# Optimization experiments

Measured on AMD Instinct MI355X. Metric: run time of the kernel, lower is better.

## Reference

```python
import jax, jax.numpy as jnp
from jax import lax
import numpy as np

B, T, K = 256, 1024, 64


def setup_inputs() -> dict:
    key = jax.random.key(0)
    k1, k2, k3 = jax.random.split(key, 3)
    emissions = jax.random.normal(k1, (B, T, K), dtype=jnp.float32)
    tag_ids = jax.random.randint(k2, (B, T), 0, K, dtype=jnp.int32)
    mask = jnp.ones((B, T), dtype=bool)
    transition_weight = jax.random.normal(k3, (K, K), dtype=jnp.float32)
    return {"emissions": emissions, "tag_ids": tag_ids, "mask": mask,
            "transition_weight": transition_weight}


def _crf_log_likelihood(emissions, tags, mask, trans):
    # emissions: [B,T,K], tags/mask: [B,T], trans: [K,K]
    maskf = mask.astype(emissions.dtype)
    # sequence score: unary emissions at gold tags + pairwise transitions
    unary = jnp.take_along_axis(emissions, tags[..., None], axis=2)[..., 0]  # [B,T]
    unary_score = jnp.sum(unary * maskf, axis=1)
    trans_score = jnp.sum(trans[tags[:, :-1], tags[:, 1:]] * maskf[:, 1:], axis=1)
    seq_score = unary_score + trans_score  # [B]
    # log partition via forward (alpha) recursion over time
    def step(alpha, xs):
        e_t, m_t = xs  # [B,K], [B]
        new = jax.nn.logsumexp(alpha[:, :, None] + trans[None], axis=1) + e_t
        alpha = jnp.where(m_t[:, None], new, alpha)  # carry through padding
        return alpha, None
    alpha0 = emissions[:, 0]
    em_t = jnp.swapaxes(emissions, 0, 1)[1:]  # [T-1,B,K]
    m_t = jnp.swapaxes(mask, 0, 1)[1:]        # [T-1,B]
    alpha, _ = lax.scan(step, alpha0, (em_t, m_t))
    log_z = jax.nn.logsumexp(alpha, axis=1)  # [B]
    return seq_score - log_z


def _crf_decode(emissions, mask, trans):
    # Viterbi: forward max recursion with backpointers, then backtrack.
    num_tags = emissions.shape[-1]
    ident = jnp.arange(num_tags, dtype=jnp.int32)[None, :]  # identity bp for padding

    def fstep(delta, xs):
        e_t, m_t = xs  # [B,K], [B]
        scores = delta[:, :, None] + trans[None]  # [B,K_prev,K_cur]
        bp = jnp.argmax(scores, axis=1).astype(jnp.int32)  # [B,K]
        new = jnp.max(scores, axis=1) + e_t
        delta = jnp.where(m_t[:, None], new, delta)
        bp = jnp.where(m_t[:, None], bp, ident)
        return delta, bp

    delta0 = emissions[:, 0]
    em_t = jnp.swapaxes(emissions, 0, 1)[1:]
    m_t = jnp.swapaxes(mask, 0, 1)[1:]
    delta, bps = lax.scan(fstep, delta0, (em_t, m_t))  # bps: [T-1,B,K]
    last_tag = jnp.argmax(delta, axis=1).astype(jnp.int32)  # [B]

    def bstep(tag, bp_t):
        prev = jnp.take_along_axis(bp_t, tag[:, None], axis=1)[:, 0]
        return prev, tag

    first_tag, tags_rest = lax.scan(bstep, last_tag, bps, reverse=True)
    decoded = jnp.concatenate([first_tag[:, None], jnp.swapaxes(tags_rest, 0, 1)], axis=1)
    return decoded  # [B,T]


def reference(emissions, tag_ids, mask, transition_weight):
    ll = _crf_log_likelihood(emissions, tag_ids, mask, transition_weight)
    loss = -jnp.mean(ll)
    decoded = _crf_decode(emissions, mask, transition_weight)
    mask_i = mask.astype(jnp.int32)
    tag_accuracy = (jnp.sum((decoded == tag_ids).astype(jnp.int32) * mask_i)
                    / jnp.sum(mask_i))
    decoded_masked = decoded * mask_i  # padded positions zeroed (ragged stand-in)
    return loss, decoded_masked, tag_accuracy
```

## Files before the change

### kernel.cpp

```cpp
#include <hip/hip_runtime.h>

#define BB 256
#define TT 1024
#define KK 64
#define CS 65


__device__ __forceinline__ float rlane(float x, int i) {
  return __int_as_float(__builtin_amdgcn_readlane(__float_as_int(x), i));
}
#define RL(S, i) rlane(S, i)

__device__ __forceinline__ float wavemax(float v) {
#pragma unroll
  for (int off = 1; off <= 32; off <<= 1) v = fmaxf(v, __shfl_xor(v, off));
  return v;
}

#define CFQ4(S, a, b, c, d) \
  q0 = __builtin_fmaf(RL(S, a), Ecol[eb + (a)], q0); \
  q1 = __builtin_fmaf(RL(S, b), Ecol[eb + (b)], q1); \
  q2 = __builtin_fmaf(RL(S, c), Ecol[eb + (c)], q2); \
  q3 = __builtin_fmaf(RL(S, d), Ecol[eb + (d)], q3);
#define CFQALL(S) \
  CFQ4(S, 0, 1, 2, 3)     CFQ4(S, 4, 5, 6, 7)     CFQ4(S, 8, 9, 10, 11) \
  CFQ4(S, 12, 13, 14, 15) CFQ4(S, 16, 17, 18, 19) CFQ4(S, 20, 21, 22, 23) \
  CFQ4(S, 24, 25, 26, 27) CFQ4(S, 28, 29, 30, 31) CFQ4(S, 32, 33, 34, 35) \
  CFQ4(S, 36, 37, 38, 39) CFQ4(S, 40, 41, 42, 43) CFQ4(S, 44, 45, 46, 47) \
  CFQ4(S, 48, 49, 50, 51) CFQ4(S, 52, 53, 54, 55) CFQ4(S, 56, 57, 58, 59) \
  CFQ4(S, 60, 61, 62, 63)

#define CFWD_STEP(T_, E_, M_) { \
  int eb = jb65; asm volatile("" : "+v"(eb)); \
  float q0 = 0.f, q1 = 0.f, q2 = 0.f, q3 = 0.f; \
  CFQALL(x) \
  float q = (q0 + q1) + (q2 + q3); \
  q *= (E_); \
  q = (M_) ? q : x; \
  if (((T_) & 7) == 0) { \
    float gm = wavemax(x); \
    q *= __builtin_amdgcn_rcpf(gm); \
    offset += __logf(gm); \
  } \
  x = q; }

#define CVQ(g, a, b, c, d) float vm##g; { \
  float v0 = RL(x, a) + Ccol[cb + (a)]; \
  float v1 = RL(x, b) + Ccol[cb + (b)]; \
  float v2 = RL(x, c) + Ccol[cb + (c)]; \
  float v3 = RL(x, d) + Ccol[cb + (d)]; \
  vm##g = fmaxf(fmaxf(v0, v1), fmaxf(v2, v3)); }

#define CVIT_STEP(T_, E_, M_) { \
  int cb = jb65; asm volatile("" : "+v"(cb)); \
  CVQ(0, 0, 1, 2, 3)      CVQ(1, 4, 5, 6, 7)      CVQ(2, 8, 9, 10, 11) \
  CVQ(3, 12, 13, 14, 15)  CVQ(4, 16, 17, 18, 19)  CVQ(5, 20, 21, 22, 23) \
  CVQ(6, 24, 25, 26, 27)  CVQ(7, 28, 29, 30, 31)  CVQ(8, 32, 33, 34, 35) \
  CVQ(9, 36, 37, 38, 39)  CVQ(10, 40, 41, 42, 43) CVQ(11, 44, 45, 46, 47) \
  CVQ(12, 48, 49, 50, 51) CVQ(13, 52, 53, 54, 55) CVQ(14, 56, 57, 58, 59) \
  CVQ(15, 60, 61, 62, 63) \
  float b0 = fmaxf(vm0, vm1),   b1 = fmaxf(vm2, vm3); \
  float b2 = fmaxf(vm4, vm5),   b3 = fmaxf(vm6, vm7); \
  float b4 = fmaxf(vm8, vm9),   b5 = fmaxf(vm10, vm11); \
  float b6 = fmaxf(vm12, vm13), b7 = fmaxf(vm14, vm15); \
  float best = fmaxf(fmaxf(fmaxf(b0, b1), fmaxf(b2, b3)), \
                     fmaxf(fmaxf(b4, b5), fmaxf(b6, b7))); \
  float nd = (M_) ? (best + (E_)) : x; \
  x = nd; }

#define AG(i0, i1, i2, i3, i4, i5, i6, i7) { \
  float v0 = RL(x2, i0) + Ccol[db + (i0)]; \
  float v1 = RL(x2, i1) + Ccol[db + (i1)]; \
  float v2 = RL(x2, i2) + Ccol[db + (i2)]; \
  float v3 = RL(x2, i3) + Ccol[db + (i3)]; \
  float v4 = RL(x2, i4) + Ccol[db + (i4)]; \
  float v5 = RL(x2, i5) + Ccol[db + (i5)]; \
  float v6 = RL(x2, i6) + Ccol[db + (i6)]; \
  float v7 = RL(x2, i7) + Ccol[db + (i7)]; \
  bool p0 = v1 > v0; float a0 = p0 ? v1 : v0; int n0 = p0 ? (i1) : (i0); \
  bool p1 = v3 > v2; float a1 = p1 ? v3 : v2; int n1 = p1 ? (i3) : (i2); \
  bool p2 = v5 > v4; float a2 = p2 ? v5 : v4; int n2 = p2 ? (i5) : (i4); \
  bool p3 = v7 > v6; float a3 = p3 ? v7 : v6; int n3 = p3 ? (i7) : (i6); \
  bool r0 = a1 > a0; float bb0 = r0 ? a1 : a0; int m0 = r0 ? n1 : n0; \
  bool r1 = a3 > a2; float bb1 = r1 ? a3 : a2; int m1 = r1 ? n3 : n2; \
  bool s0 = bb1 > bb0; float gg = s0 ? bb1 : bb0; int w0 = s0 ? m1 : m0; \
  bool u0 = gg > bv; bv = u0 ? gg : bv; bi = u0 ? w0 : bi; }

#define FG(A,B,C,D,E0,E1,E2,E3,OP) \
  "v_readlane_b32 s56, %[x], " #A "\n\t" \
  "v_readlane_b32 s57, %[x], " #B "\n\t" \
  "v_readlane_b32 s58, %[x], " #C "\n\t" \
  "v_readlane_b32 s59, %[x], " #D "\n\t" \
  #OP " v20, s56, v" #E0 "\n\t" \
  #OP " v21, s57, v" #E1 "\n\t" \
  #OP " v22, s58, v" #E2 "\n\t" \
  #OP " v23, s59, v" #E3 "\n\t"

#define FWD_DOT \
  FG(0,1,2,3,64,65,66,67,v_mul_f32)      FG(4,5,6,7,68,69,70,71,v_fmac_f32) \
  FG(8,9,10,11,72,73,74,75,v_fmac_f32)   FG(12,13,14,15,76,77,78,79,v_fmac_f32) \
  FG(16,17,18,19,80,81,82,83,v_fmac_f32) FG(20,21,22,23,84,85,86,87,v_fmac_f32) \
  FG(24,25,26,27,88,89,90,91,v_fmac_f32) FG(28,29,30,31,92,93,94,95,v_fmac_f32) \
  FG(32,33,34,35,96,97,98,99,v_fmac_f32) FG(36,37,38,39,100,101,102,103,v_fmac_f32) \
  FG(40,41,42,43,104,105,106,107,v_fmac_f32) FG(44,45,46,47,108,109,110,111,v_fmac_f32) \
  FG(48,49,50,51,112,113,114,115,v_fmac_f32) FG(52,53,54,55,116,117,118,119,v_fmac_f32) \
  FG(56,57,58,59,120,121,122,123,v_fmac_f32) FG(60,61,62,63,124,125,126,127,v_fmac_f32)

#define VG(A,B,C,D,E0,E1,E2,E3,RED) \
  "v_readlane_b32 s56, %[x], " #A "\n\t" \
  "v_readlane_b32 s57, %[x], " #B "\n\t" \
  "v_readlane_b32 s58, %[x], " #C "\n\t" \
  "v_readlane_b32 s59, %[x], " #D "\n\t" \
  "v_add_f32 v16, s56, v" #E0 "\n\t" \
  "v_add_f32 v17, s57, v" #E1 "\n\t" \
  "v_add_f32 v18, s58, v" #E2 "\n\t" \
  "v_add_f32 v19, s59, v" #E3 "\n\t" \
  "v_max3_f32 v16, v16, v17, v18\n\t" \
  RED "\n\t"

#define VIT_DOT \
  VG(0,1,2,3,64,65,66,67,"v_max_f32 v20, v16, v19") \
  VG(4,5,6,7,68,69,70,71,"v_max3_f32 v20, v20, v16, v19") \
  VG(8,9,10,11,72,73,74,75,"v_max3_f32 v20, v20, v16, v19") \
  VG(12,13,14,15,76,77,78,79,"v_max3_f32 v20, v20, v16, v19") \
  VG(16,17,18,19,80,81,82,83,"v_max3_f32 v20, v20, v16, v19") \
  VG(20,21,22,23,84,85,86,87,"v_max3_f32 v20, v20, v16, v19") \
  VG(24,25,26,27,88,89,90,91,"v_max3_f32 v20, v20, v16, v19") \
  VG(28,29,30,31,92,93,94,95,"v_max3_f32 v20, v20, v16, v19") \
  VG(32,33,34,35,96,97,98,99,"v_max3_f32 v20, v20, v16, v19") \
  VG(36,37,38,39,100,101,102,103,"v_max3_f32 v20, v20, v16, v19") \
  VG(40,41,42,43,104,105,106,107,"v_max3_f32 v20, v20, v16, v19") \
  VG(44,45,46,47,108,109,110,111,"v_max3_f32 v20, v20, v16, v19") \
  VG(48,49,50,51,112,113,114,115,"v_max3_f32 v20, v20, v16, v19") \
  VG(52,53,54,55,116,117,118,119,"v_max3_f32 v20, v20, v16, v19") \
  VG(56,57,58,59,120,121,122,123,"v_max3_f32 v20, v20, v16, v19") \
  VG(60,61,62,63,124,125,126,127,"v_max3_f32 v20, v20, v16, v19")

#define AGLD(N,OFF) "global_load_dword v" #N ", v13, %[tp] offset:" #OFF "\n\t"
#define AGLE(N,OFF) "global_load_dword v" #N ", v12, %[ep] offset:" #OFF "\n\t"
#define AGLM(N,OFF) "global_load_dword v" #N ", v14, %[mp] offset:" #OFF "\n\t"

#define ELOADS \
  AGLD(64,0) AGLD(65,256) AGLD(66,512) AGLD(67,768) AGLD(68,1024) AGLD(69,1280) \
  AGLD(70,1536) AGLD(71,1792) AGLD(72,2048) AGLD(73,2304) AGLD(74,2560) AGLD(75,2816) \
  AGLD(76,3072) AGLD(77,3328) AGLD(78,3584) AGLD(79,3840) \
  "v_add_u32 v13, 0x1000, v13\n\t" \
  AGLD(80,0) AGLD(81,256) AGLD(82,512) AGLD(83,768) AGLD(84,1024) AGLD(85,1280) \
  AGLD(86,1536) AGLD(87,1792) AGLD(88,2048) AGLD(89,2304) AGLD(90,2560) AGLD(91,2816) \
  AGLD(92,3072) AGLD(93,3328) AGLD(94,3584) AGLD(95,3840) \
  "v_add_u32 v13, 0x1000, v13\n\t" \
  AGLD(96,0) AGLD(97,256) AGLD(98,512) AGLD(99,768) AGLD(100,1024) AGLD(101,1280) \
  AGLD(102,1536) AGLD(103,1792) AGLD(104,2048) AGLD(105,2304) AGLD(106,2560) AGLD(107,2816) \
  AGLD(108,3072) AGLD(109,3328) AGLD(110,3584) AGLD(111,3840) \
  "v_add_u32 v13, 0x1000, v13\n\t" \
  AGLD(112,0) AGLD(113,256) AGLD(114,512) AGLD(115,768) AGLD(116,1024) AGLD(117,1280) \
  AGLD(118,1536) AGLD(119,1792) AGLD(120,2048) AGLD(121,2304) AGLD(122,2560) AGLD(123,2816) \
  AGLD(124,3072) AGLD(125,3328) AGLD(126,3584) AGLD(127,3840)

#define AMUL(N) "v_mul_f32 v" #N ", 0x3fb8aa3b, v" #N "\n\t"
#define AEXI(N) "v_exp_f32 v" #N ", v" #N "\n\t"
#define EEXPALL \
  AMUL(64) AMUL(65) AMUL(66) AMUL(67) AMUL(68) AMUL(69) AMUL(70) AMUL(71) \
  AMUL(72) AMUL(73) AMUL(74) AMUL(75) AMUL(76) AMUL(77) AMUL(78) AMUL(79) \
  AMUL(80) AMUL(81) AMUL(82) AMUL(83) AMUL(84) AMUL(85) AMUL(86) AMUL(87) \
  AMUL(88) AMUL(89) AMUL(90) AMUL(91) AMUL(92) AMUL(93) AMUL(94) AMUL(95) \
  AMUL(96) AMUL(97) AMUL(98) AMUL(99) AMUL(100) AMUL(101) AMUL(102) AMUL(103) \
  AMUL(104) AMUL(105) AMUL(106) AMUL(107) AMUL(108) AMUL(109) AMUL(110) AMUL(111) \
  AMUL(112) AMUL(113) AMUL(114) AMUL(115) AMUL(116) AMUL(117) AMUL(118) AMUL(119) \
  AMUL(120) AMUL(121) AMUL(122) AMUL(123) AMUL(124) AMUL(125) AMUL(126) AMUL(127) \
  AEXI(64) AEXI(65) AEXI(66) AEXI(67) AEXI(68) AEXI(69) AEXI(70) AEXI(71) \
  AEXI(72) AEXI(73) AEXI(74) AEXI(75) AEXI(76) AEXI(77) AEXI(78) AEXI(79) \
  AEXI(80) AEXI(81) AEXI(82) AEXI(83) AEXI(84) AEXI(85) AEXI(86) AEXI(87) \
  AEXI(88) AEXI(89) AEXI(90) AEXI(91) AEXI(92) AEXI(93) AEXI(94) AEXI(95) \
  AEXI(96) AEXI(97) AEXI(98) AEXI(99) AEXI(100) AEXI(101) AEXI(102) AEXI(103) \
  AEXI(104) AEXI(105) AEXI(106) AEXI(107) AEXI(108) AEXI(109) AEXI(110) AEXI(111) \
  AEXI(112) AEXI(113) AEXI(114) AEXI(115) AEXI(116) AEXI(117) AEXI(118) AEXI(119) \
  AEXI(120) AEXI(121) AEXI(122) AEXI(123) AEXI(124) AEXI(125) AEXI(126) AEXI(127)

#define EMIS16 \
  AGLE(40,0) AGLE(41,256) AGLE(42,512) AGLE(43,768) AGLE(44,1024) AGLE(45,1280) \
  AGLE(46,1536) AGLE(47,1792) AGLE(48,2048) AGLE(49,2304) AGLE(50,2560) AGLE(51,2816) \
  AGLE(52,3072) AGLE(53,3328) AGLE(54,3584) AGLE(55,3840)
#define EMIS8 \
  AGLE(40,0) AGLE(41,256) AGLE(42,512) AGLE(43,768) AGLE(44,1024) AGLE(45,1280) \
  AGLE(46,1536) AGLE(47,1792)
#define MASK16 \
  AGLM(128,0) AGLM(129,4) AGLM(130,8) AGLM(131,12) AGLM(132,16) AGLM(133,20) \
  AGLM(134,24) AGLM(135,28) AGLM(136,32) AGLM(137,36) AGLM(138,40) AGLM(139,44) \
  AGLM(140,48) AGLM(141,52) AGLM(142,56) AGLM(143,60)
#define MASK8 \
  AGLM(128,0) AGLM(129,4) AGLM(130,8) AGLM(131,12) AGLM(132,16) AGLM(133,20) \
  AGLM(134,24) AGLM(135,28)

#define AEM(D,R) "v_mul_f32 v" #D ", 0x3fb8aa3b, v" #R "\n\t"
#define EMEXP16 \
  AEM(24,40) AEM(25,41) AEM(26,42) AEM(27,43) AEM(28,44) AEM(29,45) AEM(30,46) AEM(31,47) \
  AEM(32,48) AEM(33,49) AEM(34,50) AEM(35,51) AEM(36,52) AEM(37,53) AEM(38,54) AEM(39,55) \
  AEXI(24) AEXI(25) AEXI(26) AEXI(27) AEXI(28) AEXI(29) AEXI(30) AEXI(31) \
  AEXI(32) AEXI(33) AEXI(34) AEXI(35) AEXI(36) AEXI(37) AEXI(38) AEXI(39)
#define EMEXP8 \
  AEM(24,40) AEM(25,41) AEM(26,42) AEM(27,43) AEM(28,44) AEM(29,45) AEM(30,46) AEM(31,47) \
  AEXI(24) AEXI(25) AEXI(26) AEXI(27) AEXI(28) AEXI(29) AEXI(30) AEXI(31)

#define AFSTEP(MR,EV) \
  "v_cmp_ne_u32 vcc, 0, v" #MR "\n\t" \
  FWD_DOT \
  "v_add_f32 v16, v20, v21\n\t" \
  "v_add_f32 v17, v22, v23\n\t" \
  "v_add_f32 v16, v16, v17\n\t" \
  "v_mul_f32 v16, v16, v" #EV "\n\t" \
  "v_cndmask_b32 %[x], %[x], v16, vcc\n\t"

#define RNRM \
  "v_mov_b32 v17, %[x]\n\t" \
  "ds_swizzle_b32 v18, v17 offset:0x041F\n\t" \
  "s_waitcnt lgkmcnt(0)\n\t" \
  "v_max_f32 v17, v17, v18\n\t" \
  "ds_swizzle_b32 v18, v17 offset:0x081F\n\t" \
  "s_waitcnt lgkmcnt(0)\n\t" \
  "v_max_f32 v17, v17, v18\n\t" \
  "ds_swizzle_b32 v18, v17 offset:0x101F\n\t" \
  "s_waitcnt lgkmcnt(0)\n\t" \
  "v_max_f32 v17, v17, v18\n\t" \
  "ds_swizzle_b32 v18, v17 offset:0x201F\n\t" \
  "s_waitcnt lgkmcnt(0)\n\t" \
  "v_max_f32 v17, v17, v18\n\t" \
  "ds_swizzle_b32 v18, v17 offset:0x401F\n\t" \
  "s_waitcnt lgkmcnt(0)\n\t" \
  "v_max_f32 v17, v17, v18\n\t" \
  "v_readlane_b32 s56, v17, 0\n\t" \
  "v_readlane_b32 s57, v17, 32\n\t" \
  "v_mov_b32 v18, s57\n\t" \
  "v_max_f32 v18, s56, v18\n\t" \
  "v_readlane_b32 s56, v18, 0\n\t"

#define AFSTEPR(MR,EV) \
  "v_cmp_ne_u32 vcc, 0, v" #MR "\n\t" \
  FWD_DOT \
  "v_add_f32 v16, v20, v21\n\t" \
  "v_add_f32 v17, v22, v23\n\t" \
  "v_add_f32 v16, v16, v17\n\t" \
  "v_mul_f32 v16, v16, v" #EV "\n\t" \
  RNRM \
  "v_cndmask_b32 %[x], %[x], v16, vcc\n\t" \
  "v_rcp_f32 v18, s56\n\t" \
  "v_log_f32 v19, s56\n\t" \
  "v_mul_f32 %[x], %[x], v18\n\t" \
  "v_fmac_f32 %[off], 0x3f317218, v19\n\t"

#define AVSTEP(MR,EV) \
  "v_cmp_ne_u32 vcc, 0, v" #MR "\n\t" \
  VIT_DOT \
  "v_add_f32 v16, v20, v" #EV "\n\t" \
  "v_cndmask_b32 %[x], %[x], v16, vcc\n\t"

#define CLOBS \
  "v11","v12","v13","v14","v16","v17","v18","v19","v20","v21","v22","v23", \
  "v24","v25","v26","v27","v28","v29","v30","v31","v32","v33","v34","v35", \
  "v36","v37","v38","v39","v40","v41","v42","v43","v44","v45","v46","v47", \
  "v48","v49","v50","v51","v52","v53","v54","v55", \
  "v64","v65","v66","v67","v68","v69","v70","v71","v72","v73","v74","v75", \
  "v76","v77","v78","v79","v80","v81","v82","v83","v84","v85","v86","v87", \
  "v88","v89","v90","v91","v92","v93","v94","v95","v96","v97","v98","v99", \
  "v100","v101","v102","v103","v104","v105","v106","v107","v108","v109", \
  "v110","v111","v112","v113","v114","v115","v116","v117","v118","v119", \
  "v120","v121","v122","v123","v124","v125","v126","v127","v128","v129", \
  "v130","v131","v132","v133","v134","v135","v136","v137","v138","v139", \
  "v140","v141","v142","v143", \
  "s55","s56","s57","s58","s59","vcc","scc","memory"

__global__ __launch_bounds__(512)
__attribute__((amdgpu_waves_per_eu(1, 2)))
void crf_mega_kernel(
    const float* __restrict__ em, const int* __restrict__ mask,
    const float* __restrict__ trans, const int* __restrict__ tags,
    float* __restrict__ out_dec, float* ll_sum, int* match, int* maskSum) {

  __shared__ float Ecol[KK * CS];
  __shared__ float Ccol[KK * CS];
  __shared__ __align__(16) float ckw[64][KK];
  __shared__ float fin[KK];
  __shared__ unsigned char mrow[TT];
  __shared__ unsigned char bpl[TT][KK];
  __shared__ unsigned char segm[32][KK];
  __shared__ unsigned char bs[40];
  __shared__ int redm[32];

  const int b = blockIdx.x;
  const int tid = threadIdx.x;
  const int wv = tid >> 6;
  const int j = tid & 63;
  const int jb65 = j * CS;

  const float* emb = em + (size_t)b * TT * KK;
  const int* mb = mask + (size_t)b * TT;
  const int* tgb = tags + (size_t)b * TT;

  for (int t = tid; t < TT; t += 512) mrow[t] = (unsigned char)(mb[t] ? 1 : 0);
  if (wv == 0) {
#pragma unroll 4
    for (int i = 0; i < KK; ++i) Ecol[jb65 + i] = __expf(trans[i * KK + j]);
  } else if (wv == 1) {
#pragma unroll 4
    for (int i = 0; i < KK; ++i) Ccol[jb65 + i] = trans[i * KK + j];
  }
  __syncthreads();

  if (wv == 0) {
    float raw = emb[j];
    float x, offset;
    {
      float m0 = wavemax(raw);
      offset = m0;
      float s = __expf(raw - m0);
      int eb = jb65; asm volatile("" : "+v"(eb));
      float q0 = 0.f, q1 = 0.f, q2 = 0.f, q3 = 0.f;
      CFQALL(s)
      float q = (q0 + q1) + (q2 + q3);
      q *= __expf(emb[KK + j]);
      x = mrow[1] ? q : s;
    }
    for (int t = 2; t <= 7; ++t) {
      float e = __expf(emb[(size_t)t * KK + j]);
      int m = mrow[t];
      CFWD_STEP(t, e, m)
    }
    asm volatile(
      "s_mov_b32 s55, 0\n\t"
      "v_mov_b32 v12, %[vo]\n\t"
      "v_mov_b32 v13, %[jo]\n\t"
      "v_mov_b32 v14, 32\n\t"
      ELOADS
      "s_waitcnt vmcnt(0)\n\t"
      EEXPALL
      "9:\n\t"
      MASK16
      EMIS16
      "v_add_u32 v12, 0x1000, v12\n\t"
      "v_add_u32 v14, 64, v14\n\t"
      "s_waitcnt vmcnt(0)\n\t"
      EMEXP16
      AFSTEPR(128,24) AFSTEP(129,25) AFSTEP(130,26) AFSTEP(131,27)
      AFSTEP(132,28)  AFSTEP(133,29) AFSTEP(134,30) AFSTEP(135,31)
      AFSTEPR(136,32) AFSTEP(137,33) AFSTEP(138,34) AFSTEP(139,35)
      AFSTEP(140,36)  AFSTEP(141,37) AFSTEP(142,38) AFSTEP(143,39)
      "s_add_u32 s55, s55, 1\n\t"
      "s_cmp_lt_u32 s55, 63\n\t"
      "s_cbranch_scc1 9b\n\t"
      MASK8
      EMIS8
      "s_waitcnt vmcnt(0)\n\t"
      EMEXP8
      AFSTEPR(128,24) AFSTEP(129,25) AFSTEP(130,26) AFSTEP(131,27)
      AFSTEP(132,28)  AFSTEP(133,29) AFSTEP(134,30) AFSTEP(135,31)
      "s_waitcnt vmcnt(0) lgkmcnt(0)\n\t"
      : [x]"+v"(x), [off]"+v"(offset)
      : [ep]"s"(emb), [mp]"s"(mb), [tp]"s"(trans),
        [vo]"v"(2048 + 4 * j), [jo]"v"(4 * j)
      : CLOBS);

    float ssum = x;
#pragma unroll
    for (int off = 1; off <= 32; off <<= 1) ssum += __shfl_xor(ssum, off);
    if (tid == 0) atomicAdd(ll_sum, -(offset + __logf(ssum)));

  } else if (wv == 1) {
    float x = emb[j];
    unsigned ckoff = (unsigned)(unsigned long long)(&ckw[1][j]);
    asm volatile(
      "s_mov_b32 s55, 0\n\t"
      "v_mov_b32 v11, %[ck]\n\t"
      "v_mov_b32 v12, %[vo]\n\t"
      "v_mov_b32 v13, %[jo]\n\t"
      "v_mov_b32 v14, 4\n\t"
      ELOADS
      "s_waitcnt vmcnt(0)\n\t"
      "8:\n\t"
      MASK16
      EMIS16
      "v_add_u32 v12, 0x1000, v12\n\t"
      "v_add_u32 v14, 64, v14\n\t"
      "s_waitcnt vmcnt(0)\n\t"
      AVSTEP(128,40) AVSTEP(129,41) AVSTEP(130,42) AVSTEP(131,43)
      AVSTEP(132,44) AVSTEP(133,45) AVSTEP(134,46) AVSTEP(135,47)
      AVSTEP(136,48) AVSTEP(137,49) AVSTEP(138,50) AVSTEP(139,51)
      AVSTEP(140,52) AVSTEP(141,53) AVSTEP(142,54) AVSTEP(143,55)
      "ds_write_b32 v11, %[x]\n\t"
      "v_add_u32 v11, 0x100, v11\n\t"
      "s_add_u32 s55, s55, 1\n\t"
      "s_cmp_lt_u32 s55, 63\n\t"
      "s_cbranch_scc1 8b\n\t"
      MASK8
      EMIS8
      "s_waitcnt vmcnt(0)\n\t"
      AVSTEP(128,40) AVSTEP(129,41) AVSTEP(130,42) AVSTEP(131,43)
      AVSTEP(132,44) AVSTEP(133,45) AVSTEP(134,46) AVSTEP(135,47)
      "s_waitcnt vmcnt(0) lgkmcnt(0)\n\t"
      : [x]"+v"(x)
      : [ep]"s"(emb), [mp]"s"(mb), [tp]"s"(trans),
        [vo]"v"(256 + 4 * j), [jo]"v"(4 * j), [ck]"v"(ckoff)
      : CLOBS);
    for (int t = TT - 7; t <= TT - 1; ++t) {
      float e = emb[(size_t)t * KK + j];
      int m = mrow[t];
      CVIT_STEP(t, e, m)
    }
    fin[j] = x;

  } else if (wv == 2) {
    float acc = 0.f;
    int cnt = 0;
    for (int t = j; t < TT; t += 64) {
      if (mb[t]) {
        int tg = tgb[t];
        acc += emb[(size_t)t * KK + tg];
        cnt += 1;
        if (t >= 1) acc += trans[tgb[t - 1] * KK + tg];
      }
    }
#pragma unroll
    for (int off = 1; off <= 32; off <<= 1) {
      acc += __shfl_xor(acc, off);
      cnt += __shfl_xor(cnt, off);
    }
    if (j == 0) { atomicAdd(ll_sum, acc); atomicAdd(maskSum, cnt); }
  }

  __syncthreads();

#pragma unroll 1
  for (int kk = 0; kk < 4; ++kk) {
    int s = wv + 8 * kk;
    int tS = 32 * s + 1;
    int tE = (s == 31) ? (TT - 1) : (32 * s + 32);
    float x2 = (s == 0) ? emb[j] : ckw[2 * s][j];
    float e_nx = emb[(size_t)tS * KK + j];
#pragma unroll 1
    for (int t = tS; t <= tE; ++t) {
      float e = e_nx;
      if (t < tE) e_nx = emb[(size_t)(t + 1) * KK + j];
      int db = jb65; asm volatile("" : "+v"(db));
      float bv = -__builtin_inff(); int bi = 0;
      AG(0, 1, 2, 3, 4, 5, 6, 7)        AG(8, 9, 10, 11, 12, 13, 14, 15)
      AG(16, 17, 18, 19, 20, 21, 22, 23) AG(24, 25, 26, 27, 28, 29, 30, 31)
      AG(32, 33, 34, 35, 36, 37, 38, 39) AG(40, 41, 42, 43, 44, 45, 46, 47)
      AG(48, 49, 50, 51, 52, 53, 54, 55) AG(56, 57, 58, 59, 60, 61, 62, 63)
      int m = mrow[t];
      float nd = m ? (bv + e) : x2;
      int bp = m ? bi : j;
      bpl[t][j] = (unsigned char)bp;
      x2 = nd;
    }
  }
  __syncthreads();

  {
    int j0 = tid & 63;
    int sg = tid >> 6;
    int xs[4]; int tS[4], tE[4];
#pragma unroll
    for (int kk = 0; kk < 4; ++kk) {
      int s = sg + 8 * kk;
      xs[kk] = j0;
      tS[kk] = 32 * s + 1;
      tE[kk] = (s == 31) ? (TT - 1) : (32 * s + 32);
    }
    for (int q = 0; q < 32; ++q) {
#pragma unroll
      for (int kk = 0; kk < 4; ++kk) {
        int t = tE[kk] - q;
        if (t >= tS[kk]) xs[kk] = bpl[t][xs[kk]];
      }
    }
#pragma unroll
    for (int kk = 0; kk < 4; ++kk) segm[sg + 8 * kk][j0] = (unsigned char)xs[kk];
  }
  __syncthreads();

  if (tid == 0) {
    float bd = fin[0];
    int lt = 0;
    for (int i = 1; i < KK; ++i) {
      float v2 = fin[i];
      if (v2 > bd) { bd = v2; lt = i; }
    }
    bs[32] = (unsigned char)lt;
    for (int s = 31; s >= 0; --s) bs[s] = segm[s][bs[s + 1]];
  }
  __syncthreads();

  if (tid < 32) {
    int s = tid;
    int x = bs[s + 1];
    int cnt = 0;
    int tEnd = (s == 31) ? (TT - 1) : (32 * s + 32);
    if (s == 31) {
      int m = mrow[TT - 1];
      out_dec[(size_t)b * TT + TT - 1] = (float)(m ? x : 0);
      cnt += (m && x == tgb[TT - 1]);
    }
    for (int t = tEnd; t >= 32 * s + 1; --t) {
      x = bpl[t][x];
      int m2 = mrow[t - 1];
      out_dec[(size_t)b * TT + t - 1] = (float)(m2 ? x : 0);
      cnt += (m2 && x == tgb[t - 1]);
    }
    redm[s] = cnt;
  }
  __syncthreads();
  if (tid == 0) {
    int c = 0;
    for (int s = 0; s < 32; ++s) c += redm[s];
    atomicAdd(match, c);
  }
}

__global__ void finalize_kernel(const float* ll_sum, const int* match,
                                const int* maskSum, float* d_out) {
  d_out[0] = -(*ll_sum) / (float)BB;
  d_out[1 + BB * TT] = (float)(*match) / (float)(*maskSum);
}

extern "C" void kernel_launch(void* const* d_in, const int* in_sizes, int n_in,
                              void* d_out, int out_size, void* d_ws, size_t ws_size,
                              hipStream_t stream) {
  const float* em = (const float*)d_in[0];
  const int* tags = (const int*)d_in[1];
  const int* mask = (const int*)d_in[2];
  const float* trans = (const float*)d_in[3];
  float* out = (float*)d_out;

  float* ll_sum = (float*)d_ws;
  int* match = (int*)((char*)d_ws + 4);
  int* maskSum = (int*)((char*)d_ws + 8);

  hipMemsetAsync(d_ws, 0, 12, stream);
  crf_mega_kernel<<<BB, 512, 0, stream>>>(em, mask, trans, tags, out + 1,
                                          ll_sum, match, maskSum);
  finalize_kernel<<<1, 1, 0, stream>>>(ll_sum, match, maskSum, out);
}
```

Before: 588.8 us.

## Software-pipeline emission/mask loads and batch readlanes in CRF recurrences

```diff
diff --git a/kernel.cpp b/kernel.cpp
--- a/kernel.cpp
+++ b/kernel.cpp
@@ -86,55 +86,104 @@
   bool s0 = bb1 > bb0; float gg = s0 ? bb1 : bb0; int w0 = s0 ? m1 : m0; \
   bool u0 = gg > bv; bv = u0 ? gg : bv; bi = u0 ? w0 : bi; }
 
-#define FG(A,B,C,D,E0,E1,E2,E3,OP) \
-  "v_readlane_b32 s56, %[x], " #A "\n\t" \
-  "v_readlane_b32 s57, %[x], " #B "\n\t" \
-  "v_readlane_b32 s58, %[x], " #C "\n\t" \
-  "v_readlane_b32 s59, %[x], " #D "\n\t" \
-  #OP " v20, s56, v" #E0 "\n\t" \
-  #OP " v21, s57, v" #E1 "\n\t" \
-  #OP " v22, s58, v" #E2 "\n\t" \
-  #OP " v23, s59, v" #E3 "\n\t"
-
-#define FWD_DOT \
-  FG(0,1,2,3,64,65,66,67,v_mul_f32)      FG(4,5,6,7,68,69,70,71,v_fmac_f32) \
-  FG(8,9,10,11,72,73,74,75,v_fmac_f32)   FG(12,13,14,15,76,77,78,79,v_fmac_f32) \
-  FG(16,17,18,19,80,81,82,83,v_fmac_f32) FG(20,21,22,23,84,85,86,87,v_fmac_f32) \
-  FG(24,25,26,27,88,89,90,91,v_fmac_f32) FG(28,29,30,31,92,93,94,95,v_fmac_f32) \
-  FG(32,33,34,35,96,97,98,99,v_fmac_f32) FG(36,37,38,39,100,101,102,103,v_fmac_f32) \
-  FG(40,41,42,43,104,105,106,107,v_fmac_f32) FG(44,45,46,47,108,109,110,111,v_fmac_f32) \
-  FG(48,49,50,51,112,113,114,115,v_fmac_f32) FG(52,53,54,55,116,117,118,119,v_fmac_f32) \
-  FG(56,57,58,59,120,121,122,123,v_fmac_f32) FG(60,61,62,63,124,125,126,127,v_fmac_f32)
-
-#define VG(A,B,C,D,E0,E1,E2,E3,RED) \
-  "v_readlane_b32 s56, %[x], " #A "\n\t" \
-  "v_readlane_b32 s57, %[x], " #B "\n\t" \
-  "v_readlane_b32 s58, %[x], " #C "\n\t" \
-  "v_readlane_b32 s59, %[x], " #D "\n\t" \
-  "v_add_f32 v16, s56, v" #E0 "\n\t" \
-  "v_add_f32 v17, s57, v" #E1 "\n\t" \
-  "v_add_f32 v18, s58, v" #E2 "\n\t" \
-  "v_add_f32 v19, s59, v" #E3 "\n\t" \
+#define RLA(a,b,c,d,e,f,g,h) \
+  "v_readlane_b32 s36, %[x], " #a "\n\t" \
+  "v_readlane_b32 s37, %[x], " #b "\n\t" \
+  "v_readlane_b32 s38, %[x], " #c "\n\t" \
+  "v_readlane_b32 s39, %[x], " #d "\n\t" \
+  "v_readlane_b32 s40, %[x], " #e "\n\t" \
+  "v_readlane_b32 s41, %[x], " #f "\n\t" \
+  "v_readlane_b32 s42, %[x], " #g "\n\t" \
+  "v_readlane_b32 s43, %[x], " #h "\n\t"
+#define RLB(a,b,c,d,e,f,g,h) \
+  "v_readlane_b32 s44, %[x], " #a "\n\t" \
+  "v_readlane_b32 s45, %[x], " #b "\n\t" \
+  "v_readlane_b32 s46, %[x], " #c "\n\t" \
+  "v_readlane_b32 s47, %[x], " #d "\n\t" \
+  "v_readlane_b32 s48, %[x], " #e "\n\t" \
+  "v_readlane_b32 s49, %[x], " #f "\n\t" \
+  "v_readlane_b32 s50, %[x], " #g "\n\t" \
+  "v_readlane_b32 s51, %[x], " #h "\n\t"
+
+#define FMA8F(E0,E1,E2,E3,E4,E5,E6,E7) \
+  "v_mul_f32 v20, s36, v" #E0 "\n\t" \
+  "v_mul_f32 v21, s37, v" #E1 "\n\t" \
+  "v_mul_f32 v22, s38, v" #E2 "\n\t" \
+  "v_mul_f32 v23, s39, v" #E3 "\n\t" \
+  "v_fmac_f32 v20, s40, v" #E4 "\n\t" \
+  "v_fmac_f32 v21, s41, v" #E5 "\n\t" \
+  "v_fmac_f32 v22, s42, v" #E6 "\n\t" \
+  "v_fmac_f32 v23, s43, v" #E7 "\n\t"
+#define FMA8A(E0,E1,E2,E3,E4,E5,E6,E7) \
+  "v_fmac_f32 v20, s36, v" #E0 "\n\t" \
+  "v_fmac_f32 v21, s37, v" #E1 "\n\t" \
+  "v_fmac_f32 v22, s38, v" #E2 "\n\t" \
+  "v_fmac_f32 v23, s39, v" #E3 "\n\t" \
+  "v_fmac_f32 v20, s40, v" #E4 "\n\t" \
+  "v_fmac_f32 v21, s41, v" #E5 "\n\t" \
+  "v_fmac_f32 v22, s42, v" #E6 "\n\t" \
+  "v_fmac_f32 v23, s43, v" #E7 "\n\t"
+#define FMA8B(E0,E1,E2,E3,E4,E5,E6,E7) \
+  "v_fmac_f32 v20, s44, v" #E0 "\n\t" \
+  "v_fmac_f32 v21, s45, v" #E1 "\n\t" \
+  "v_fmac_f32 v22, s46, v" #E2 "\n\t" \
+  "v_fmac_f32 v23, s47, v" #E3 "\n\t" \
+  "v_fmac_f32 v20, s48, v" #E4 "\n\t" \
+  "v_fmac_f32 v21, s49, v" #E5 "\n\t" \
+  "v_fmac_f32 v22, s50, v" #E6 "\n\t" \
+  "v_fmac_f32 v23, s51, v" #E7 "\n\t"
+
+#define FWD_DOT_P \
+  RLA(0,1,2,3,4,5,6,7) \
+  RLB(8,9,10,11,12,13,14,15) \
+  FMA8F(64,65,66,67,68,69,70,71) \
+  RLA(16,17,18,19,20,21,22,23) \
+  FMA8B(72,73,74,75,76,77,78,79) \
+  RLB(24,25,26,27,28,29,30,31) \
+  FMA8A(80,81,82,83,84,85,86,87) \
+  RLA(32,33,34,35,36,37,38,39) \
+  FMA8B(88,89,90,91,92,93,94,95) \
+  RLB(40,41,42,43,44,45,46,47) \
+  FMA8A(96,97,98,99,100,101,102,103) \
+  RLA(48,49,50,51,52,53,54,55) \
+  FMA8B(104,105,106,107,108,109,110,111) \
+  RLB(56,57,58,59,60,61,62,63) \
+  FMA8A(112,113,114,115,116,117,118,119) \
+  FMA8B(120,121,122,123,124,125,126,127)
+
+#define VG4(S0,S1,S2,S3,E0,E1,E2,E3,RED) \
+  "v_add_f32 v16, " #S0 ", v" #E0 "\n\t" \
+  "v_add_f32 v17, " #S1 ", v" #E1 "\n\t" \
+  "v_add_f32 v18, " #S2 ", v" #E2 "\n\t" \
+  "v_add_f32 v19, " #S3 ", v" #E3 "\n\t" \
   "v_max3_f32 v16, v16, v17, v18\n\t" \
   RED "\n\t"
 
-#define VIT_DOT \
-  VG(0,1,2,3,64,65,66,67,"v_max_f32 v20, v16, v19") \
-  VG(4,5,6,7,68,69,70,71,"v_max3_f32 v20, v20, v16, v19") \
-  VG(8,9,10,11,72,73,74,75,"v_max3_f32 v20, v20, v16, v19") \
-  VG(12,13,14,15,76,77,78,79,"v_max3_f32 v20, v20, v16, v19") \
-  VG(16,17,18,19,80,81,82,83,"v_max3_f32 v20, v20, v16, v19") \
-  VG(20,21,22,23,84,85,86,87,"v_max3_f32 v20, v20, v16, v19") \
-  VG(24,25,26,27,88,89,90,91,"v_max3_f32 v20, v20, v16, v19") \
-  VG(28,29,30,31,92,93,94,95,"v_max3_f32 v20, v20, v16, v19") \
-  VG(32,33,34,35,96,97,98,99,"v_max3_f32 v20, v20, v16, v19") \
-  VG(36,37,38,39,100,101,102,103,"v_max3_f32 v20, v20, v16, v19") \
-  VG(40,41,42,43,104,105,106,107,"v_max3_f32 v20, v20, v16, v19") \
-  VG(44,45,46,47,108,109,110,111,"v_max3_f32 v20, v20, v16, v19") \
-  VG(48,49,50,51,112,113,114,115,"v_max3_f32 v20, v20, v16, v19") \
-  VG(52,53,54,55,116,117,118,119,"v_max3_f32 v20, v20, v16, v19") \
-  VG(56,57,58,59,120,121,122,123,"v_max3_f32 v20, v20, v16, v19") \
-  VG(60,61,62,63,124,125,126,127,"v_max3_f32 v20, v20, v16, v19")
+#define VIT_DOT_P \
+  RLA(0,1,2,3,4,5,6,7) \
+  RLB(8,9,10,11,12,13,14,15) \
+  VG4(s36,s37,s38,s39,64,65,66,67,"v_max_f32 v20, v16, v19") \
+  VG4(s40,s41,s42,s43,68,69,70,71,"v_max3_f32 v20, v20, v16, v19") \
+  RLA(16,17,18,19,20,21,22,23) \
+  VG4(s44,s45,s46,s47,72,73,74,75,"v_max3_f32 v20, v20, v16, v19") \
+  VG4(s48,s49,s50,s51,76,77,78,79,"v_max3_f32 v20, v20, v16, v19") \
+  RLB(24,25,26,27,28,29,30,31) \
+  VG4(s36,s37,s38,s39,80,81,82,83,"v_max3_f32 v20, v20, v16, v19") \
+  VG4(s40,s41,s42,s43,84,85,86,87,"v_max3_f32 v20, v20, v16, v19") \
+  RLA(32,33,34,35,36,37,38,39) \
+  VG4(s44,s45,s46,s47,88,89,90,91,"v_max3_f32 v20, v20, v16, v19") \
+  VG4(s48,s49,s50,s51,92,93,94,95,"v_max3_f32 v20, v20, v16, v19") \
+  RLB(40,41,42,43,44,45,46,47) \
+  VG4(s36,s37,s38,s39,96,97,98,99,"v_max3_f32 v20, v20, v16, v19") \
+  VG4(s40,s41,s42,s43,100,101,102,103,"v_max3_f32 v20, v20, v16, v19") \
+  RLA(48,49,50,51,52,53,54,55) \
+  VG4(s44,s45,s46,s47,104,105,106,107,"v_max3_f32 v20, v20, v16, v19") \
+  VG4(s48,s49,s50,s51,108,109,110,111,"v_max3_f32 v20, v20, v16, v19") \
+  RLB(56,57,58,59,60,61,62,63) \
+  VG4(s36,s37,s38,s39,112,113,114,115,"v_max3_f32 v20, v20, v16, v19") \
+  VG4(s40,s41,s42,s43,116,117,118,119,"v_max3_f32 v20, v20, v16, v19") \
+  VG4(s44,s45,s46,s47,120,121,122,123,"v_max3_f32 v20, v20, v16, v19") \
+  VG4(s48,s49,s50,s51,124,125,126,127,"v_max3_f32 v20, v20, v16, v19")
 
 #define AGLD(N,OFF) "global_load_dword v" #N ", v13, %[tp] offset:" #OFF "\n\t"
 #define AGLE(N,OFF) "global_load_dword v" #N ", v12, %[ep] offset:" #OFF "\n\t"
@@ -184,13 +233,39 @@
 #define EMIS8 \
   AGLE(40,0) AGLE(41,256) AGLE(42,512) AGLE(43,768) AGLE(44,1024) AGLE(45,1280) \
   AGLE(46,1536) AGLE(47,1792)
+#define EMIS16B \
+  AGLE(24,0) AGLE(25,256) AGLE(26,512) AGLE(27,768) AGLE(28,1024) AGLE(29,1280) \
+  AGLE(30,1536) AGLE(31,1792) AGLE(32,2048) AGLE(33,2304) AGLE(34,2560) AGLE(35,2816) \
+  AGLE(36,3072) AGLE(37,3328) AGLE(38,3584) AGLE(39,3840)
+#define EMIS8B \
+  AGLE(24,0) AGLE(25,256) AGLE(26,512) AGLE(27,768) AGLE(28,1024) AGLE(29,1280) \
+  AGLE(30,1536) AGLE(31,1792)
 #define MASK16 \
   AGLM(128,0) AGLM(129,4) AGLM(130,8) AGLM(131,12) AGLM(132,16) AGLM(133,20) \
   AGLM(134,24) AGLM(135,28) AGLM(136,32) AGLM(137,36) AGLM(138,40) AGLM(139,44) \
   AGLM(140,48) AGLM(141,52) AGLM(142,56) AGLM(143,60)
-#define MASK8 \
-  AGLM(128,0) AGLM(129,4) AGLM(130,8) AGLM(131,12) AGLM(132,16) AGLM(133,20) \
-  AGLM(134,24) AGLM(135,28)
+#define MASK16B \
+  AGLM(144,0) AGLM(145,4) AGLM(146,8) AGLM(147,12) AGLM(148,16) AGLM(149,20) \
+  AGLM(150,24) AGLM(151,28) AGLM(152,32) AGLM(153,36) AGLM(154,40) AGLM(155,44) \
+  AGLM(156,48) AGLM(157,52) AGLM(158,56) AGLM(159,60)
+#define MASK8B \
+  AGLM(144,0) AGLM(145,4) AGLM(146,8) AGLM(147,12) AGLM(148,16) AGLM(149,20) \
+  AGLM(150,24) AGLM(151,28)
+
+#define MOVMSK \
+  "v_mov_b32 v128, v144\n\tv_mov_b32 v129, v145\n\tv_mov_b32 v130, v146\n\t" \
+  "v_mov_b32 v131, v147\n\tv_mov_b32 v132, v148\n\tv_mov_b32 v133, v149\n\t" \
+  "v_mov_b32 v134, v150\n\tv_mov_b32 v135, v151\n\tv_mov_b32 v136, v152\n\t" \
+  "v_mov_b32 v137, v153\n\tv_mov_b32 v138, v154\n\tv_mov_b32 v139, v155\n\t" \
+  "v_mov_b32 v140, v156\n\tv_mov_b32 v141, v157\n\tv_mov_b32 v142, v158\n\t" \
+  "v_mov_b32 v143, v159\n\t"
+#define MOVEMI \
+  "v_mov_b32 v40, v24\n\tv_mov_b32 v41, v25\n\tv_mov_b32 v42, v26\n\t" \
+  "v_mov_b32 v43, v27\n\tv_mov_b32 v44, v28\n\tv_mov_b32 v45, v29\n\t" \
+  "v_mov_b32 v46, v30\n\tv_mov_b32 v47, v31\n\tv_mov_b32 v48, v32\n\t" \
+  "v_mov_b32 v49, v33\n\tv_mov_b32 v50, v34\n\tv_mov_b32 v51, v35\n\t" \
+  "v_mov_b32 v52, v36\n\tv_mov_b32 v53, v37\n\tv_mov_b32 v54, v38\n\t" \
+  "v_mov_b32 v55, v39\n\t"
 
 #define AEM(D,R) "v_mul_f32 v" #D ", 0x3fb8aa3b, v" #R "\n\t"
 #define EMEXP16 \
@@ -202,9 +277,9 @@
   AEM(24,40) AEM(25,41) AEM(26,42) AEM(27,43) AEM(28,44) AEM(29,45) AEM(30,46) AEM(31,47) \
   AEXI(24) AEXI(25) AEXI(26) AEXI(27) AEXI(28) AEXI(29) AEXI(30) AEXI(31)
 
-#define AFSTEP(MR,EV) \
+#define AFSTEP_P(MR,EV) \
   "v_cmp_ne_u32 vcc, 0, v" #MR "\n\t" \
-  FWD_DOT \
+  FWD_DOT_P \
   "v_add_f32 v16, v20, v21\n\t" \
   "v_add_f32 v17, v22, v23\n\t" \
   "v_add_f32 v16, v16, v17\n\t" \
@@ -234,9 +309,9 @@
   "v_max_f32 v18, s56, v18\n\t" \
   "v_readlane_b32 s56, v18, 0\n\t"
 
-#define AFSTEPR(MR,EV) \
+#define AFSTEPR_P(MR,EV) \
   "v_cmp_ne_u32 vcc, 0, v" #MR "\n\t" \
-  FWD_DOT \
+  FWD_DOT_P \
   "v_add_f32 v16, v20, v21\n\t" \
   "v_add_f32 v17, v22, v23\n\t" \
   "v_add_f32 v16, v16, v17\n\t" \
@@ -248,11 +323,22 @@
   "v_mul_f32 %[x], %[x], v18\n\t" \
   "v_fmac_f32 %[off], 0x3f317218, v19\n\t"
 
-#define AVSTEP(MR,EV) \
+#define AVSTEP_P(MR,EV) \
   "v_cmp_ne_u32 vcc, 0, v" #MR "\n\t" \
-  VIT_DOT \
+  VIT_DOT_P \
   "v_add_f32 v16, v20, v" #EV "\n\t" \
   "v_cndmask_b32 %[x], %[x], v16, vcc\n\t"
+
+#define FSTEPS16 \
+  AFSTEPR_P(128,24) AFSTEP_P(129,25) AFSTEP_P(130,26) AFSTEP_P(131,27) \
+  AFSTEP_P(132,28)  AFSTEP_P(133,29) AFSTEP_P(134,30) AFSTEP_P(135,31) \
+  AFSTEPR_P(136,32) AFSTEP_P(137,33) AFSTEP_P(138,34) AFSTEP_P(139,35) \
+  AFSTEP_P(140,36)  AFSTEP_P(141,37) AFSTEP_P(142,38) AFSTEP_P(143,39)
+#define VSTEPS16 \
+  AVSTEP_P(128,40) AVSTEP_P(129,41) AVSTEP_P(130,42) AVSTEP_P(131,43) \
+  AVSTEP_P(132,44) AVSTEP_P(133,45) AVSTEP_P(134,46) AVSTEP_P(135,47) \
+  AVSTEP_P(136,48) AVSTEP_P(137,49) AVSTEP_P(138,50) AVSTEP_P(139,51) \
+  AVSTEP_P(140,52) AVSTEP_P(141,53) AVSTEP_P(142,54) AVSTEP_P(143,55)
 
 #define CLOBS \
   "v11","v12","v13","v14","v16","v17","v18","v19","v20","v21","v22","v23", \
@@ -266,8 +352,10 @@
   "v110","v111","v112","v113","v114","v115","v116","v117","v118","v119", \
   "v120","v121","v122","v123","v124","v125","v126","v127","v128","v129", \
   "v130","v131","v132","v133","v134","v135","v136","v137","v138","v139", \
-  "v140","v141","v142","v143", \
-  "s55","s56","s57","s58","s59","vcc","scc","memory"
+  "v140","v141","v142","v143","v144","v145","v146","v147","v148","v149", \
+  "v150","v151","v152","v153","v154","v155","v156","v157","v158","v159", \
+  "s36","s37","s38","s39","s40","s41","s42","s43","s44","s45","s46","s47", \
+  "s48","s49","s50","s51","s55","s56","s57","s58","s59","vcc","scc","memory"
 
 __global__ __launch_bounds__(512)
 __attribute__((amdgpu_waves_per_eu(1, 2)))
@@ -331,28 +419,32 @@
       "v_mov_b32 v13, %[jo]\n\t"
       "v_mov_b32 v14, 32\n\t"
       ELOADS
+      MASK16
+      EMIS16
       "s_waitcnt vmcnt(0)\n\t"
       EEXPALL
       "9:\n\t"
-      MASK16
+      EMEXP16
+      "v_add_u32 v12, 0x1000, v12\n\t"
       EMIS16
+      "v_add_u32 v14, 64, v14\n\t"
+      MASK16B
+      FSTEPS16
+      "s_waitcnt vmcnt(0)\n\t"
+      MOVMSK
+      "s_add_u32 s55, s55, 1\n\t"
+      "s_cmp_lt_u32 s55, 62\n\t"
+      "s_cbranch_scc1 9b\n\t"
+      EMEXP16
       "v_add_u32 v12, 0x1000, v12\n\t"
+      EMIS8
       "v_add_u32 v14, 64, v14\n\t"
-      "s_waitcnt vmcnt(0)\n\t"
-      EMEXP16
-      AFSTEPR(128,24) AFSTEP(129,25) AFSTEP(130,26) AFSTEP(131,27)
-      AFSTEP(132,28)  AFSTEP(133,29) AFSTEP(134,30) AFSTEP(135,31)
-      AFSTEPR(136,32) AFSTEP(137,33) AFSTEP(138,34) AFSTEP(139,35)
-      AFSTEP(140,36)  AFSTEP(141,37) AFSTEP(142,38) AFSTEP(143,39)
-      "s_add_u32 s55, s55, 1\n\t"
-      "s_cmp_lt_u32 s55, 63\n\t"
-      "s_cbranch_scc1 9b\n\t"
-      MASK8
-      EMIS8
+      MASK8B
+      FSTEPS16
       "s_waitcnt vmcnt(0)\n\t"
       EMEXP8
-      AFSTEPR(128,24) AFSTEP(129,25) AFSTEP(130,26) AFSTEP(131,27)
-      AFSTEP(132,28)  AFSTEP(133,29) AFSTEP(134,30) AFSTEP(135,31)
+      AFSTEPR_P(144,24) AFSTEP_P(145,25) AFSTEP_P(146,26) AFSTEP_P(147,27)
+      AFSTEP_P(148,28)  AFSTEP_P(149,29) AFSTEP_P(150,30) AFSTEP_P(151,31)
       "s_waitcnt vmcnt(0) lgkmcnt(0)\n\t"
       : [x]"+v"(x), [off]"+v"(offset)
       : [ep]"s"(emb), [mp]"s"(mb), [tp]"s"(trans),
@@ -374,27 +466,32 @@
       "v_mov_b32 v13, %[jo]\n\t"
       "v_mov_b32 v14, 4\n\t"
       ELOADS
+      MASK16
+      EMIS16
       "s_waitcnt vmcnt(0)\n\t"
       "8:\n\t"
-      MASK16
-      EMIS16
       "v_add_u32 v12, 0x1000, v12\n\t"
+      EMIS16B
       "v_add_u32 v14, 64, v14\n\t"
-      "s_waitcnt vmcnt(0)\n\t"
-      AVSTEP(128,40) AVSTEP(129,41) AVSTEP(130,42) AVSTEP(131,43)
-      AVSTEP(132,44) AVSTEP(133,45) AVSTEP(134,46) AVSTEP(135,47)
-      AVSTEP(136,48) AVSTEP(137,49) AVSTEP(138,50) AVSTEP(139,51)
-      AVSTEP(140,52) AVSTEP(141,53) AVSTEP(142,54) AVSTEP(143,55)
+      MASK16B
+      VSTEPS16
       "ds_write_b32 v11, %[x]\n\t"
       "v_add_u32 v11, 0x100, v11\n\t"
+      "s_waitcnt vmcnt(0)\n\t"
+      MOVEMI
+      MOVMSK
       "s_add_u32 s55, s55, 1\n\t"
-      "s_cmp_lt_u32 s55, 63\n\t"
+      "s_cmp_lt_u32 s55, 62\n\t"
       "s_cbranch_scc1 8b\n\t"
-      MASK8
-      EMIS8
+      "v_add_u32 v12, 0x1000, v12\n\t"
+      EMIS8B
+      "v_add_u32 v14, 64, v14\n\t"
+      MASK8B
+      VSTEPS16
+      "ds_write_b32 v11, %[x]\n\t"
       "s_waitcnt vmcnt(0)\n\t"
-      AVSTEP(128,40) AVSTEP(129,41) AVSTEP(130,42) AVSTEP(131,43)
-      AVSTEP(132,44) AVSTEP(133,45) AVSTEP(134,46) AVSTEP(135,47)
+      AVSTEP_P(144,24) AVSTEP_P(145,25) AVSTEP_P(146,26) AVSTEP_P(147,27)
+      AVSTEP_P(148,28) AVSTEP_P(149,29) AVSTEP_P(150,30) AVSTEP_P(151,31)
       "s_waitcnt vmcnt(0) lgkmcnt(0)\n\t"
       : [x]"+v"(x)
       : [ep]"s"(emb), [mp]"s"(mb), [tp]"s"(trans),
```

Result: slower. 601.2 us (+2.1%).
